# Performance work log

Hardware: AMD Instinct MI355X
Metric: run time of the kernel (lower is better)

Reference implementation:

```python
import jax, jax.numpy as jnp
import numpy as np

DIMS = [3, 64, 64, 64, 3]  # [input_dim] + hidden dims + [input_dim]
TOTAL_W = sum(DIMS[l] * DIMS[l + 1] + 4 * DIMS[l + 1] for l in range(len(DIMS) - 1))  # 9356


def setup_inputs() -> dict:
    key = jax.random.key(0)
    k1, k2, k3 = jax.random.split(key, 3)
    B, N = 64, 8192
    context = jax.random.normal(k1, (B, N), dtype=jnp.float32)
    y = jax.random.normal(k2, (B, N, DIMS[0]), dtype=jnp.float32)
    tnw = jax.random.normal(k3, (B, TOTAL_W), dtype=jnp.float32) * 0.1
    return {"context": context, "y": y, "target_networks_weights": tnw}


def reference(context, y, target_networks_weights):
    B = target_networks_weights.shape[0]
    dx = y  # [B, N, dims[0]]
    i = 0
    n_layers = len(DIMS) - 1
    for l in range(n_layers):
        dl, dl1 = DIMS[l], DIMS[l + 1]
        W = target_networks_weights[:, i:i + dl * dl1].reshape(B, dl, dl1)
        i += dl * dl1
        bias = target_networks_weights[:, i:i + dl1]          # [B, dl1]
        i += dl1
        w_scale = target_networks_weights[:, i:i + dl1]        # [B, dl1]
        i += dl1
        b_scale = target_networks_weights[:, i:i + dl1]        # [B, dl1]
        i += dl1
        w_shift = target_networks_weights[:, i:i + dl1]        # [B, dl1]
        i += dl1
        # batched matmul + bias
        dx = jnp.einsum('bnd,bde->bne', dx, W) + bias[:, None, :]
        # sigmoid gate: bmm(context[:, :, None], w_scale[:, None, :]) = outer product
        scale = jax.nn.sigmoid(context[:, :, None] * w_scale[:, None, :] + b_scale[:, None, :])
        dx = scale * dx
        # shift term
        dx = dx + context[:, :, None] * w_shift[:, None, :]
        if l < n_layers - 1:
            dx = jax.nn.softplus(dx)
    return dx
```

## Files before the change

### kernel.cpp

```cpp
#include <hip/hip_runtime.h>
#include <math.h>

#define BB 64
#define NN 8192
#define TOTAL_W 9356

typedef _Float16 f16x4 __attribute__((ext_vector_type(4)));
typedef float f32x4 __attribute__((ext_vector_type(4)));
typedef float f32x2 __attribute__((ext_vector_type(2)));
typedef unsigned int u32x2 __attribute__((ext_vector_type(2)));

#define L2E 1.44269504088896340736f
#define LN2 0.6931471805599453f

#define WS_FILM 0
#define WS_A1   4096
#define WS_A2   12288
#define WS_A0   20480
#define WS_A3   22528
#define WSB     24576

#define FILM2_OFF 0
#define A1_OFF    4096
#define A2_OFF    12288
#define LDS_BYTES 20480

#if __has_builtin(__builtin_amdgcn_mfma_f32_16x16x16_f16)
#define MFMAK16(a, b, c) __builtin_amdgcn_mfma_f32_16x16x16_f16(a, b, c, 0, 0, 0)
#else
#define MFMAK16(a, b, c) __builtin_amdgcn_mfma_f32_16x16x16f16(a, b, c, 0, 0, 0)
#endif
#define EXP2 __builtin_amdgcn_exp2f
#define LOG2 __builtin_amdgcn_logf
#define RCPF __builtin_amdgcn_rcpf

__device__ __forceinline__ f32x2 pfma(f32x2 a, f32x2 b, f32x2 c) {
  return __builtin_elementwise_fma(a, b, c);
}

__device__ __forceinline__ const f32x4* film_base(const unsigned char* smem, int l, int qd) {
  return (const f32x4*)(smem + FILM2_OFF + ((l * 16 + qd) << 6));
}

template<bool SP>
__device__ __forceinline__ f16x4 film_quad(f32x4 acc, float ctx,
                                           f32x4 wscq, f32x4 bscq, f32x4 wshq) {
  f32x2 ctx2 = {ctx, ctx};
  f32x2 one = {1.f, 1.f};
  f32x2 z0 = pfma(ctx2, (f32x2){wscq.x, wscq.y}, (f32x2){bscq.x, bscq.y});
  f32x2 z1 = pfma(ctx2, (f32x2){wscq.z, wscq.w}, (f32x2){bscq.z, bscq.w});
  f32x2 d0 = {EXP2(-z0.x), EXP2(-z0.y)};  d0 += one;
  f32x2 d1 = {EXP2(-z1.x), EXP2(-z1.y)};  d1 += one;
  f32x2 s0 = {RCPF(d0.x), RCPF(d0.y)};
  f32x2 s1 = {RCPF(d1.x), RCPF(d1.y)};
  f32x2 v0 = pfma(ctx2, (f32x2){wshq.x, wshq.y}, s0 * (f32x2){acc.x, acc.y});
  f32x2 v1 = pfma(ctx2, (f32x2){wshq.z, wshq.w}, s1 * (f32x2){acc.z, acc.w});
  if (SP) {
    f32x2 l2 = {L2E, L2E}, ln = {LN2, LN2};
    f32x2 t0 = v0 * l2, t1 = v1 * l2;
    f32x2 u0 = {EXP2(t0.x), EXP2(t0.y)};  u0 += one;
    f32x2 u1 = {EXP2(t1.x), EXP2(t1.y)};  u1 += one;
    f32x2 g0 = {LOG2(u0.x), LOG2(u0.y)};
    f32x2 g1 = {LOG2(u1.x), LOG2(u1.y)};
    v0 = g0 * ln;
    v1 = g1 * ln;
  }
  auto p01 = __builtin_amdgcn_cvt_pkrtz(v0.x, v0.y);
  auto p23 = __builtin_amdgcn_cvt_pkrtz(v1.x, v1.y);
  u32x2 w;
  w.x = __builtin_bit_cast(unsigned int, p01);
  w.y = __builtin_bit_cast(unsigned int, p23);
  return __builtin_bit_cast(f16x4, w);
}

__device__ __forceinline__ f16x4 a_tile(const unsigned char* smem, int aoff,
                                        int m, int t, int lane) {
  return *(const f16x4*)(smem + aoff + (((m * 4 + t) * 64 + lane) << 3));
}

__global__ __launch_bounds__(512)
void ode_prep_kernel(const float* __restrict__ tnw, unsigned char* __restrict__ ws) {
  const int b = blockIdx.x;
  const int tid = threadIdx.x;
  const float* __restrict__ wb = tnw + (size_t)b * TOTAL_W;
  unsigned char* __restrict__ wsb = ws + (size_t)b * WSB;

  if (tid < 64) {
    const int biaso[4] = {192, 4544, 8896, 9344};
    const int dim[4] = {64, 64, 64, 3};
#pragma unroll
    for (int l = 0; l < 4; ++l) {
      float bv = 0.f, wscv = 0.f, bscv = 0.f, wshv = 0.f;
      if (tid < dim[l]) {
        int bo = biaso[l], d = dim[l];
        bv = wb[bo + tid];
        wscv = wb[bo + d + tid] * L2E;
        bscv = wb[bo + 2 * d + tid] * L2E;
        wshv = wb[bo + 3 * d + tid];
      }
      float* f2 = (float*)(wsb + WS_FILM + ((l * 16 + (tid >> 2)) << 6)) + (tid & 3);
      f2[0] = bv;
      f2[4] = wscv;
      f2[8] = bscv;
      f2[12] = wshv;
    }
  }
#pragma unroll
  for (int L = 0; L < 2; ++L) {
    const int woff = L ? 4800 : 448;
    unsigned char* dst = wsb + (L ? WS_A2 : WS_A1);
#pragma unroll
    for (int it = 0; it < 2; ++it) {
      int idx = tid + it * 512;
      int lane = idx & 63;
      int tile = idx >> 6;
      int m = tile >> 2, t = tile & 3;
      int f_out = 16 * m + (lane & 15);
      int f_in0 = 16 * t + 4 * (lane >> 4);
      f16x4 h;
#pragma unroll
      for (int i = 0; i < 4; ++i) h[i] = (_Float16)wb[woff + (f_in0 + i) * 64 + f_out];
      *(f16x4*)(dst + idx * 8) = h;
    }
  }
  if (tid < 256) {
    int m = tid >> 6;
    int lane = tid & 63;
    int kg = lane >> 4, row = lane & 15;
    f16x4 h = {0, 0, 0, 0};
    if (kg == 0) {
#pragma unroll
      for (int i = 0; i < 3; ++i) h[i] = (_Float16)wb[i * 64 + 16 * m + row];
    }
    *(f16x4*)(wsb + WS_A0 + tid * 8) = h;
  }
  if (tid < 256) {
    int t = tid >> 6;
    int lane = tid & 63;
    int kg = lane >> 4, row = lane & 15;
    f16x4 h = {0, 0, 0, 0};
    if (row < 3) {
#pragma unroll
      for (int i = 0; i < 4; ++i)
        h[i] = (_Float16)wb[9152 + (16 * t + 4 * kg + i) * 3 + row];
    }
    *(f16x4*)(wsb + WS_A3 + tid * 8) = h;
  }
}

__global__ __launch_bounds__(256)
void ode_hypernet_kernel(const float* __restrict__ context,
                         const float* __restrict__ y,
                         const unsigned char* __restrict__ ws,
                         float* __restrict__ out) {
  __shared__ __align__(16) unsigned char smem[LDS_BYTES];
  const int b = blockIdx.y;
  const int tid = threadIdx.x;
  const unsigned char* __restrict__ wsb = ws + (size_t)b * WSB;

  const int lane = tid & 63;
  const int wid = tid >> 6;
  const int g = lane >> 4;
  const int col = lane & 15;

#pragma unroll
  for (int it = 0; it < 5; ++it) {
    int i = tid + it * 256;
    *(f32x4*)(smem + i * 16) = *(const f32x4*)(wsb + i * 16);
  }
  f16x4 A0r[4], A3r[4];
#pragma unroll
  for (int m = 0; m < 4; ++m)
    A0r[m] = *(const f16x4*)(wsb + WS_A0 + ((m * 64 + lane) << 3));
#pragma unroll
  for (int t = 0; t < 4; ++t)
    A3r[t] = *(const f16x4*)(wsb + WS_A3 + ((t * 64 + lane) << 3));
  __syncthreads();

  const int pt0 = wid * 32 + col;
  const int nb = blockIdx.x * 256;
  const size_t cb = (size_t)b * NN;

  float ctxs[4], yv[4][3];
#pragma unroll
  for (int k = 0; k < 4; ++k) {
    int n = nb + (k >> 1) * 128 + pt0 + (k & 1) * 16;
    ctxs[k] = context[cb + n];
    const float* yp = y + (cb + n) * 3;
    yv[k][0] = yp[0]; yv[k][1] = yp[1]; yv[k][2] = yp[2];
  }

#pragma unroll
  for (int ss = 0; ss < 2; ++ss) {
    const float ctx0 = ctxs[ss * 2], ctx1 = ctxs[ss * 2 + 1];
    const int n0 = nb + ss * 128 + pt0;
    const int n1 = n0 + 16;

    f16x4 By0 = {0, 0, 0, 0}, By1 = {0, 0, 0, 0};
    if (g == 0) {
      By0[0] = (_Float16)yv[ss * 2][0];
      By0[1] = (_Float16)yv[ss * 2][1];
      By0[2] = (_Float16)yv[ss * 2][2];
      By1[0] = (_Float16)yv[ss * 2 + 1][0];
      By1[1] = (_Float16)yv[ss * 2 + 1][1];
      By1[2] = (_Float16)yv[ss * 2 + 1][2];
    }

    f16x4 Bc0[4], Bc1[4], Bd0[4], Bd1[4];

#pragma unroll
    for (int m = 0; m < 4; ++m) {
      const f32x4* fb = film_base(smem, 0, 4 * m + g);
      f32x4 biasq = fb[0], wscq = fb[1], bscq = fb[2], wshq = fb[3];
      f32x4 c0 = biasq, c1 = biasq;
      c0 = MFMAK16(A0r[m], By0, c0);
      c1 = MFMAK16(A0r[m], By1, c1);
      Bc0[m] = film_quad<true>(c0, ctx0, wscq, bscq, wshq);
      Bc1[m] = film_quad<true>(c1, ctx1, wscq, bscq, wshq);
    }

#pragma unroll
    for (int m = 0; m < 4; ++m) {
      const f32x4* fb = film_base(smem, 1, 4 * m + g);
      f32x4 biasq = fb[0], wscq = fb[1], bscq = fb[2], wshq = fb[3];
      f32x4 c0 = biasq, c1 = biasq;
#pragma unroll
      for (int t = 0; t < 4; ++t) {
        f16x4 a = a_tile(smem, A1_OFF, m, t, lane);
        c0 = MFMAK16(a, Bc0[t], c0);
        c1 = MFMAK16(a, Bc1[t], c1);
      }
      Bd0[m] = film_quad<true>(c0, ctx0, wscq, bscq, wshq);
      Bd1[m] = film_quad<true>(c1, ctx1, wscq, bscq, wshq);
    }

#pragma unroll
    for (int m = 0; m < 4; ++m) {
      const f32x4* fb = film_base(smem, 2, 4 * m + g);
      f32x4 biasq = fb[0], wscq = fb[1], bscq = fb[2], wshq = fb[3];
      f32x4 c0 = biasq, c1 = biasq;
#pragma unroll
      for (int t = 0; t < 4; ++t) {
        f16x4 a = a_tile(smem, A2_OFF, m, t, lane);
        c0 = MFMAK16(a, Bd0[t], c0);
        c1 = MFMAK16(a, Bd1[t], c1);
      }
      Bc0[m] = film_quad<true>(c0, ctx0, wscq, bscq, wshq);
      Bc1[m] = film_quad<true>(c1, ctx1, wscq, bscq, wshq);
    }

    {
      const f32x4* fb = film_base(smem, 3, g);
      f32x4 biasq = fb[0], wscq = fb[1], bscq = fb[2], wshq = fb[3];
      f32x4 c0 = biasq, c1 = biasq;
#pragma unroll
      for (int t = 0; t < 4; ++t) {
        c0 = MFMAK16(A3r[t], Bc0[t], c0);
        c1 = MFMAK16(A3r[t], Bc1[t], c1);
      }
      if (g == 0) {
#pragma unroll
        for (int p = 0; p < 2; ++p) {
          f32x4 c = p ? c1 : c0;
          float ctx = p ? ctx1 : ctx0;
          int n = p ? n1 : n0;
#pragma unroll
          for (int j = 0; j < 3; ++j) {
            float z = fmaf(ctx, wscq[j], bscq[j]);
            float s = RCPF(1.0f + EXP2(-z));
            float v = fmaf(ctx, wshq[j], s * c[j]);
            out[((size_t)b * NN + n) * 3 + j] = v;
          }
        }
      }
    }
  }
}

extern "C" void kernel_launch(void* const* d_in, const int* in_sizes, int n_in,
                              void* d_out, int out_size, void* d_ws, size_t ws_size,
                              hipStream_t stream) {
  const float* context = (const float*)d_in[0];
  const float* y       = (const float*)d_in[1];
  const float* tnw     = (const float*)d_in[2];
  float* out           = (float*)d_out;
  unsigned char* ws    = (unsigned char*)d_ws;

  ode_prep_kernel<<<dim3(BB, 1, 1), dim3(512, 1, 1), 0, stream>>>(tnw, ws);
  dim3 grid(NN / 256, BB, 1);
  dim3 block(256, 1, 1);
  ode_hypernet_kernel<<<grid, block, 0, stream>>>(context, y, ws, out);
}
```

Before: 56.08 us.

## Fold log2/ln2 constants into weights and process four point groups per layer

Premultiplies bias, shift and weights by log2(e) (and the last-layer weights by ln2) in the prep kernel, so softplus runs directly in base-2 without the per-element scale multiplies. The main kernel also moves from two sequential passes of two point groups to a single pass over all four groups per layer. That loads each A tile and FiLM parameter once per layer instead of twice and gives the MFMA and transcendental work more independent chains to interleave. In exchange it raises register pressure (Bc/Bd now hold 32 f16x4 values), which could lower occupancy or cause spills.

```diff
diff --git a/kernel.cpp b/kernel.cpp
--- a/kernel.cpp
+++ b/kernel.cpp
@@ -56,14 +56,10 @@
   f32x2 v0 = pfma(ctx2, (f32x2){wshq.x, wshq.y}, s0 * (f32x2){acc.x, acc.y});
   f32x2 v1 = pfma(ctx2, (f32x2){wshq.z, wshq.w}, s1 * (f32x2){acc.z, acc.w});
   if (SP) {
-    f32x2 l2 = {L2E, L2E}, ln = {LN2, LN2};
-    f32x2 t0 = v0 * l2, t1 = v1 * l2;
-    f32x2 u0 = {EXP2(t0.x), EXP2(t0.y)};  u0 += one;
-    f32x2 u1 = {EXP2(t1.x), EXP2(t1.y)};  u1 += one;
-    f32x2 g0 = {LOG2(u0.x), LOG2(u0.y)};
-    f32x2 g1 = {LOG2(u1.x), LOG2(u1.y)};
-    v0 = g0 * ln;
-    v1 = g1 * ln;
+    f32x2 u0 = {EXP2(v0.x), EXP2(v0.y)};  u0 += one;
+    f32x2 u1 = {EXP2(v1.x), EXP2(v1.y)};  u1 += one;
+    v0 = (f32x2){LOG2(u0.x), LOG2(u0.y)};
+    v1 = (f32x2){LOG2(u1.x), LOG2(u1.y)};
   }
   auto p01 = __builtin_amdgcn_cvt_pkrtz(v0.x, v0.y);
   auto p23 = __builtin_amdgcn_cvt_pkrtz(v1.x, v1.y);
@@ -93,10 +89,11 @@
       float bv = 0.f, wscv = 0.f, bscv = 0.f, wshv = 0.f;
       if (tid < dim[l]) {
         int bo = biaso[l], d = dim[l];
-        bv = wb[bo + tid];
+        float bs = (l < 3) ? L2E : 1.0f;
+        bv = wb[bo + tid] * bs;
         wscv = wb[bo + d + tid] * L2E;
         bscv = wb[bo + 2 * d + tid] * L2E;
-        wshv = wb[bo + 3 * d + tid];
+        wshv = wb[bo + 3 * d + tid] * bs;
       }
       float* f2 = (float*)(wsb + WS_FILM + ((l * 16 + (tid >> 2)) << 6)) + (tid & 3);
       f2[0] = bv;
@@ -130,7 +127,7 @@
     f16x4 h = {0, 0, 0, 0};
     if (kg == 0) {
 #pragma unroll
-      for (int i = 0; i < 3; ++i) h[i] = (_Float16)wb[i * 64 + 16 * m + row];
+      for (int i = 0; i < 3; ++i) h[i] = (_Float16)(wb[i * 64 + 16 * m + row] * L2E);
     }
     *(f16x4*)(wsb + WS_A0 + tid * 8) = h;
   }
@@ -142,7 +139,7 @@
     if (row < 3) {
 #pragma unroll
       for (int i = 0; i < 4; ++i)
-        h[i] = (_Float16)wb[9152 + (16 * t + 4 * kg + i) * 3 + row];
+        h[i] = (_Float16)(wb[9152 + (16 * t + 4 * kg + i) * 3 + row] * LN2);
     }
     *(f16x4*)(wsb + WS_A3 + tid * 8) = h;
   }
@@ -181,96 +178,85 @@
   const int nb = blockIdx.x * 256;
   const size_t cb = (size_t)b * NN;
 
-  float ctxs[4], yv[4][3];
+  float ctxs[4];
+  f16x4 By[4];
 #pragma unroll
   for (int k = 0; k < 4; ++k) {
     int n = nb + (k >> 1) * 128 + pt0 + (k & 1) * 16;
     ctxs[k] = context[cb + n];
     const float* yp = y + (cb + n) * 3;
-    yv[k][0] = yp[0]; yv[k][1] = yp[1]; yv[k][2] = yp[2];
-  }
-
-#pragma unroll
-  for (int ss = 0; ss < 2; ++ss) {
-    const float ctx0 = ctxs[ss * 2], ctx1 = ctxs[ss * 2 + 1];
-    const int n0 = nb + ss * 128 + pt0;
-    const int n1 = n0 + 16;
-
-    f16x4 By0 = {0, 0, 0, 0}, By1 = {0, 0, 0, 0};
+    f16x4 v = {0, 0, 0, 0};
     if (g == 0) {
-      By0[0] = (_Float16)yv[ss * 2][0];
-      By0[1] = (_Float16)yv[ss * 2][1];
-      By0[2] = (_Float16)yv[ss * 2][2];
-      By1[0] = (_Float16)yv[ss * 2 + 1][0];
-      By1[1] = (_Float16)yv[ss * 2 + 1][1];
-      By1[2] = (_Float16)yv[ss * 2 + 1][2];
-    }
-
-    f16x4 Bc0[4], Bc1[4], Bd0[4], Bd1[4];
-
-#pragma unroll
-    for (int m = 0; m < 4; ++m) {
-      const f32x4* fb = film_base(smem, 0, 4 * m + g);
-      f32x4 biasq = fb[0], wscq = fb[1], bscq = fb[2], wshq = fb[3];
-      f32x4 c0 = biasq, c1 = biasq;
-      c0 = MFMAK16(A0r[m], By0, c0);
-      c1 = MFMAK16(A0r[m], By1, c1);
-      Bc0[m] = film_quad<true>(c0, ctx0, wscq, bscq, wshq);
-      Bc1[m] = film_quad<true>(c1, ctx1, wscq, bscq, wshq);
-    }
-
-#pragma unroll
-    for (int m = 0; m < 4; ++m) {
-      const f32x4* fb = film_base(smem, 1, 4 * m + g);
-      f32x4 biasq = fb[0], wscq = fb[1], bscq = fb[2], wshq = fb[3];
-      f32x4 c0 = biasq, c1 = biasq;
-#pragma unroll
-      for (int t = 0; t < 4; ++t) {
-        f16x4 a = a_tile(smem, A1_OFF, m, t, lane);
-        c0 = MFMAK16(a, Bc0[t], c0);
-        c1 = MFMAK16(a, Bc1[t], c1);
-      }
-      Bd0[m] = film_quad<true>(c0, ctx0, wscq, bscq, wshq);
-      Bd1[m] = film_quad<true>(c1, ctx1, wscq, bscq, wshq);
-    }
-
-#pragma unroll
-    for (int m = 0; m < 4; ++m) {
-      const f32x4* fb = film_base(smem, 2, 4 * m + g);
-      f32x4 biasq = fb[0], wscq = fb[1], bscq = fb[2], wshq = fb[3];
-      f32x4 c0 = biasq, c1 = biasq;
-#pragma unroll
-      for (int t = 0; t < 4; ++t) {
-        f16x4 a = a_tile(smem, A2_OFF, m, t, lane);
-        c0 = MFMAK16(a, Bd0[t], c0);
-        c1 = MFMAK16(a, Bd1[t], c1);
-      }
-      Bc0[m] = film_quad<true>(c0, ctx0, wscq, bscq, wshq);
-      Bc1[m] = film_quad<true>(c1, ctx1, wscq, bscq, wshq);
-    }
-
-    {
-      const f32x4* fb = film_base(smem, 3, g);
-      f32x4 biasq = fb[0], wscq = fb[1], bscq = fb[2], wshq = fb[3];
-      f32x4 c0 = biasq, c1 = biasq;
-#pragma unroll
-      for (int t = 0; t < 4; ++t) {
-        c0 = MFMAK16(A3r[t], Bc0[t], c0);
-        c1 = MFMAK16(A3r[t], Bc1[t], c1);
-      }
+      v[0] = (_Float16)yp[0];
+      v[1] = (_Float16)yp[1];
+      v[2] = (_Float16)yp[2];
+    }
+    By[k] = v;
+  }
+
+  f16x4 Bc[4][4], Bd[4][4];
+
+#pragma unroll
+  for (int m = 0; m < 4; ++m) {
+    const f32x4* fb = film_base(smem, 0, 4 * m + g);
+    f32x4 biasq = fb[0], wscq = fb[1], bscq = fb[2], wshq = fb[3];
+#pragma unroll
+    for (int k = 0; k < 4; ++k) {
+      f32x4 c = biasq;
+      c = MFMAK16(A0r[m], By[k], c);
+      Bc[k][m] = film_quad<true>(c, ctxs[k], wscq, bscq, wshq);
+    }
+  }
+
+#pragma unroll
+  for (int m = 0; m < 4; ++m) {
+    const f32x4* fb = film_base(smem, 1, 4 * m + g);
+    f32x4 biasq = fb[0], wscq = fb[1], bscq = fb[2], wshq = fb[3];
+    f16x4 a[4];
+#pragma unroll
+    for (int t = 0; t < 4; ++t) a[t] = a_tile(smem, A1_OFF, m, t, lane);
+#pragma unroll
+    for (int k = 0; k < 4; ++k) {
+      f32x4 c = biasq;
+#pragma unroll
+      for (int t = 0; t < 4; ++t) c = MFMAK16(a[t], Bc[k][t], c);
+      Bd[k][m] = film_quad<true>(c, ctxs[k], wscq, bscq, wshq);
+    }
+  }
+
+#pragma unroll
+  for (int m = 0; m < 4; ++m) {
+    const f32x4* fb = film_base(smem, 2, 4 * m + g);
+    f32x4 biasq = fb[0], wscq = fb[1], bscq = fb[2], wshq = fb[3];
+    f16x4 a[4];
+#pragma unroll
+    for (int t = 0; t < 4; ++t) a[t] = a_tile(smem, A2_OFF, m, t, lane);
+#pragma unroll
+    for (int k = 0; k < 4; ++k) {
+      f32x4 c = biasq;
+#pragma unroll
+      for (int t = 0; t < 4; ++t) c = MFMAK16(a[t], Bd[k][t], c);
+      Bc[k][m] = film_quad<true>(c, ctxs[k], wscq, bscq, wshq);
+    }
+  }
+
+  {
+    const f32x4* fb = film_base(smem, 3, g);
+    f32x4 biasq = fb[0], wscq = fb[1], bscq = fb[2], wshq = fb[3];
+#pragma unroll
+    for (int k = 0; k < 4; ++k) {
+      f32x4 c = biasq;
+#pragma unroll
+      for (int t = 0; t < 4; ++t) c = MFMAK16(A3r[t], Bc[k][t], c);
       if (g == 0) {
-#pragma unroll
-        for (int p = 0; p < 2; ++p) {
-          f32x4 c = p ? c1 : c0;
-          float ctx = p ? ctx1 : ctx0;
-          int n = p ? n1 : n0;
-#pragma unroll
-          for (int j = 0; j < 3; ++j) {
-            float z = fmaf(ctx, wscq[j], bscq[j]);
-            float s = RCPF(1.0f + EXP2(-z));
-            float v = fmaf(ctx, wshq[j], s * c[j]);
-            out[((size_t)b * NN + n) * 3 + j] = v;
-          }
+        int n = nb + (k >> 1) * 128 + pt0 + (k & 1) * 16;
+        float ctx = ctxs[k];
+#pragma unroll
+        for (int j = 0; j < 3; ++j) {
+          float z = fmaf(ctx, wscq[j], bscq[j]);
+          float s = RCPF(1.0f + EXP2(-z));
+          float v = fmaf(ctx, wshq[j], s * c[j]);
+          out[((size_t)b * NN + n) * 3 + j] = v;
         }
       }
     }
```

After: 55.31 us. About the same (-1.4%).
